# Performance work log

Measured on AMD Instinct MI355X. Metric: run time of the kernel, lower is better.

Reference implementation:

```python
import jax, jax.numpy as jnp
import numpy as np

TOP_K = 2
EPS = 1e-6

def setup_inputs() -> dict:
    key = jax.random.key(0)
    ks = jax.random.split(key, 4)
    B, L, D, E, ED = 2, 2048, 2048, 8, 2048
    scale_gu = (6.0 / D) ** 0.5   # kaiming_uniform-ish bound
    scale_dn = (6.0 / ED) ** 0.5
    return {
        "x": jax.random.normal(ks[0], (B, L, D), jnp.float32),
        "router_scale": jnp.ones((D,), jnp.float32),
        "gate_w": jax.random.normal(ks[1], (D, E), jnp.float32) * (D ** -0.5),
        "gate_up": jax.random.uniform(ks[2], (E, D, 2 * ED), jnp.float32, -scale_gu, scale_gu),
        "down": jax.random.uniform(ks[3], (E, ED, D), jnp.float32, -scale_dn, scale_dn),
        "per_expert_scale": jnp.ones((E,), jnp.float32),
    }

def reference(x, router_scale, gate_w, gate_up, down, per_expert_scale):
    B, L, D = x.shape
    E = gate_up.shape[0]
    # --- Router: RMSNorm (no scale) * D^-0.5 * router_scale -> linear -> softmax -> topk -> renorm
    h = x * jax.lax.rsqrt(jnp.mean(x * x, axis=-1, keepdims=True) + EPS)
    h = h * (D ** -0.5) * router_scale
    logits = (h @ gate_w).astype(jnp.float32)            # [B,L,E]
    probs = jax.nn.softmax(logits, axis=-1)
    w, idx = jax.lax.top_k(probs, TOP_K)                 # [B,L,K]
    w = w / jnp.clip(jnp.sum(w, axis=-1, keepdims=True), 1e-12)
    w = w.astype(x.dtype)
    # --- Experts: dense compute over all experts, weighted combine by routing
    N = B * L
    xf = x.reshape(N, D)
    idxf = idx.reshape(N, TOP_K)
    wf = w.reshape(N, TOP_K)
    # combine[n,e] = sum_k wf[n,k] * (idxf[n,k]==e); top_k indices are distinct per token
    combine = jnp.zeros((N, E), x.dtype).at[jnp.arange(N)[:, None], idxf].add(wf)
    hh = jnp.einsum('nd,edf->nef', xf, gate_up)          # [N,E,2*ED]
    gate, up = jnp.split(hh, 2, axis=-1)
    act = jax.nn.gelu(gate, approximate=False) * up      # [N,E,ED]
    y = jnp.einsum('nef,efd->ned', act, down)            # [N,E,D]
    out = jnp.einsum('ne,ned->nd', combine * per_expert_scale, y)
    return out.reshape(B, L, D)
```

## Files before the change

### kernel.cpp

```cpp
#include <hip/hip_runtime.h>
#include <hip/hip_bf16.h>
#include <math.h>

#define NTOK 4096
#define DM   2048
#define NE   8
#define BK   64

using f32x4  = float __attribute__((ext_vector_type(4)));
using bf16x8 = __bf16 __attribute__((ext_vector_type(8)));
using u32x4  = unsigned int __attribute__((ext_vector_type(4)));

__device__ __forceinline__ unsigned short bf16bits(float f){
  unsigned u = __builtin_bit_cast(unsigned, f);
  return (unsigned short)((u + 0x7fffu + ((u >> 16) & 1u)) >> 16);
}

__device__ __forceinline__ void load_lds16(const void* g, void* l){
  __builtin_amdgcn_global_load_lds(
      (const __attribute__((address_space(1))) unsigned int*)g,
      (__attribute__((address_space(3))) unsigned int*)l, 16, 0, 0);
}

__global__ __launch_bounds__(256) void router_kernel(
    const float* __restrict__ x, const float* __restrict__ rs,
    const float* __restrict__ gw, const float* __restrict__ pes,
    unsigned short* __restrict__ xbf, int* __restrict__ cnt,
    int* __restrict__ toklist, float* __restrict__ slotw)
{
  const int wv = threadIdx.x >> 6, l = threadIdx.x & 63;
  const int n = blockIdx.x * 4 + wv;
  const float* xr = x + (size_t)n * DM;
  unsigned short* xb = xbf + (size_t)n * DM;
  float ssq = 0.f;
  float lg[8] = {0,0,0,0,0,0,0,0};
  #pragma unroll
  for (int q = 0; q < 8; ++q){
    int c4 = l + 64 * q;
    float4 v = ((const float4*)xr)[c4];
    float4 r = ((const float4*)rs)[c4];
    ssq += v.x*v.x + v.y*v.y + v.z*v.z + v.w*v.w;
    ushort4 o; o.x = bf16bits(v.x); o.y = bf16bits(v.y); o.z = bf16bits(v.z); o.w = bf16bits(v.w);
    ((ushort4*)xb)[c4] = o;
    float xs0 = v.x*r.x, xs1 = v.y*r.y, xs2 = v.z*r.z, xs3 = v.w*r.w;
    const float4* gp = (const float4*)(gw + (size_t)c4 * 32);
    float4 ga, gb;
    ga = gp[0]; gb = gp[1];
    lg[0]+=xs0*ga.x; lg[1]+=xs0*ga.y; lg[2]+=xs0*ga.z; lg[3]+=xs0*ga.w;
    lg[4]+=xs0*gb.x; lg[5]+=xs0*gb.y; lg[6]+=xs0*gb.z; lg[7]+=xs0*gb.w;
    ga = gp[2]; gb = gp[3];
    lg[0]+=xs1*ga.x; lg[1]+=xs1*ga.y; lg[2]+=xs1*ga.z; lg[3]+=xs1*ga.w;
    lg[4]+=xs1*gb.x; lg[5]+=xs1*gb.y; lg[6]+=xs1*gb.z; lg[7]+=xs1*gb.w;
    ga = gp[4]; gb = gp[5];
    lg[0]+=xs2*ga.x; lg[1]+=xs2*ga.y; lg[2]+=xs2*ga.z; lg[3]+=xs2*ga.w;
    lg[4]+=xs2*gb.x; lg[5]+=xs2*gb.y; lg[6]+=xs2*gb.z; lg[7]+=xs2*gb.w;
    ga = gp[6]; gb = gp[7];
    lg[0]+=xs3*ga.x; lg[1]+=xs3*ga.y; lg[2]+=xs3*ga.z; lg[3]+=xs3*ga.w;
    lg[4]+=xs3*gb.x; lg[5]+=xs3*gb.y; lg[6]+=xs3*gb.z; lg[7]+=xs3*gb.w;
  }
  #pragma unroll
  for (int off = 32; off; off >>= 1){
    ssq += __shfl_xor(ssq, off, 64);
    #pragma unroll
    for (int e2 = 0; e2 < 8; ++e2) lg[e2] += __shfl_xor(lg[e2], off, 64);
  }
  if (l == 0){
    float c = rsqrtf(ssq * (1.0f/DM) + 1e-6f) * 0.022097086912079608f;
    float mx = -1e30f;
    #pragma unroll
    for (int e2 = 0; e2 < 8; ++e2){ lg[e2] *= c; mx = fmaxf(mx, lg[e2]); }
    float l0 = lg[0]; int i0 = 0;
    #pragma unroll
    for (int e2 = 1; e2 < 8; ++e2) if (lg[e2] > l0){ l0 = lg[e2]; i0 = e2; }
    int i1 = (i0 == 0) ? 1 : 0; float l1 = (i0 == 0) ? lg[1] : lg[0];
    #pragma unroll
    for (int e2 = 0; e2 < 8; ++e2){ if (e2 != i0 && lg[e2] > l1){ l1 = lg[e2]; i1 = e2; } }
    float p0 = expf(l0 - mx), p1 = expf(l1 - mx);
    float sw = fmaxf(p0 + p1, 1e-12f);
    float w0 = p0 / sw, w1 = p1 / sw;
    int s0 = atomicAdd(&cnt[i0], 1);
    toklist[i0 * NTOK + s0] = n;
    slotw[i0 * NTOK + s0] = w0 * pes[i0];
    int s1 = atomicAdd(&cnt[i1], 1);
    toklist[i1 * NTOK + s1] = n;
    slotw[i1 * NTOK + s1] = w1 * pes[i1];
  }
}

__global__ void scan_kernel(const int* __restrict__ cnt, int* __restrict__ basep){
  if (threadIdx.x == 0){
    int a = 0;
    for (int e = 0; e < NE; ++e){ basep[e] = a; a += cnt[e]; }
  }
}

__global__ __launch_bounds__(256) void conv_transpose_kernel(
    const float* __restrict__ W, unsigned short* __restrict__ Wt, int ncols)
{
  const int z = blockIdx.z;
  const float* src = W + (size_t)z * 2048 * ncols;
  unsigned short* dst = Wt + (size_t)z * ncols * 2048;
  const int n0 = blockIdx.x * 64, k0 = blockIdx.y * 64;
  __shared__ __align__(16) unsigned short t[64][72];
  const int tid = threadIdx.x;
  const int kl = tid >> 4;
  const int nl = (tid & 15) * 4;
  #pragma unroll
  for (int q = 0; q < 4; ++q){
    int k = kl + q * 16;
    float4 v = *(const float4*)(src + (size_t)(k0 + k) * ncols + n0 + nl);
    t[nl+0][k] = bf16bits(v.x);
    t[nl+1][k] = bf16bits(v.y);
    t[nl+2][k] = bf16bits(v.z);
    t[nl+3][k] = bf16bits(v.w);
  }
  __syncthreads();
  const int nr = tid >> 3;
  const int k8 = (tid & 7) * 8;
  #pragma unroll
  for (int q = 0; q < 2; ++q){
    int n = nr + q * 32;
    u32x4 v = *(const u32x4*)&t[n][k8];
    *(u32x4*)(dst + (size_t)(n0 + n) * 2048 + k0 + k8) = v;
  }
}

template<int MODE>
__global__ __launch_bounds__(256, 4) void moe_gemm(
    const unsigned short* __restrict__ Abuf,
    const unsigned short* __restrict__ Wt,
    unsigned short* __restrict__ act,
    float* __restrict__ out,
    const int* __restrict__ cnt,
    const int* __restrict__ basep,
    const int* __restrict__ toklist,
    const float* __restrict__ slotw,
    int e0)
{
  int e, fbi, m0;
  if (gridDim.z == NE){
    int flat = blockIdx.x + gridDim.x * (blockIdx.y + 32 * blockIdx.z);
    e = e0 + (flat & 7);
    int Mreal = (cnt[e] + 127) >> 7;
    int j = flat >> 3;
    if (j >= Mreal * (int)gridDim.x) return;
    m0 = (j % Mreal) * 128;
    fbi = j / Mreal;
  } else {
    e = e0 + blockIdx.z;
    m0 = blockIdx.y * 128;
    fbi = blockIdx.x;
  }
  const int z = e - e0;
  const int ce = cnt[e];
  if (m0 >= ce) return;
  const int tid = threadIdx.x;
  const int l = tid & 63;
  const int wv = tid >> 6;
  const int wr = wv >> 1, wc = wv & 1;
  const int baseE = basep[e];
  const size_t ncols = (MODE == 0) ? 4096 : 2048;
  const unsigned short* Wz = Wt + (size_t)z * ncols * 2048;

  __shared__ __align__(16) unsigned short As[128 * BK];
  __shared__ __align__(16) unsigned short Bs[128 * BK];
  __shared__ unsigned char diagpad[MODE ? 544 : 16];
  if (basep[0] == -1) *(volatile unsigned char*)&diagpad[tid & 15] = 1;

  const unsigned short* asrc[4];
  const unsigned short* bsrc[4];
  #pragma unroll
  for (int q = 0; q < 4; ++q){
    int row = q * 32 + (tid >> 3);
    int g = (tid & 7) ^ (row & 7);
    long rs;
    if (MODE == 0) rs = toklist[e * NTOK + min(m0 + row, ce - 1)];
    else           rs = baseE + min(m0 + row, ce - 1);
    asrc[q] = Abuf + (size_t)rs * 2048 + g * 8;
    int wcol;
    if (MODE == 0) wcol = (row < 64) ? (fbi * 64 + row) : (2048 + fbi * 64 + row - 64);
    else           wcol = fbi * 128 + row;
    bsrc[q] = Wz + (size_t)wcol * 2048 + g * 8;
  }

  f32x4 acc[4][4];
  #pragma unroll
  for (int i = 0; i < 4; ++i)
    #pragma unroll
    for (int j2 = 0; j2 < 4; ++j2)
      acc[i][j2] = (f32x4){0.f, 0.f, 0.f, 0.f};

  const int aoff0 = (wr * 64 + (l & 15)) * BK;
  int boffs[4];
  if (MODE == 0){
    boffs[0] = (wc * 32 + (l & 15)) * BK;
    boffs[1] = (wc * 32 + 16 + (l & 15)) * BK;
    boffs[2] = (64 + wc * 32 + (l & 15)) * BK;
    boffs[3] = (64 + wc * 32 + 16 + (l & 15)) * BK;
  } else {
    #pragma unroll
    for (int ni = 0; ni < 4; ++ni) boffs[ni] = (wc * 64 + ni * 16 + (l & 15)) * BK;
  }
  const int lsw = l & 7;
  const int lq = l >> 4;

  #pragma unroll 1
  for (int k0 = 0; k0 < 2048; k0 += BK){
    if (k0) __syncthreads();
    #pragma unroll
    for (int q = 0; q < 4; ++q)
      load_lds16(asrc[q] + k0, &As[q * 2048 + wv * 512]);
    #pragma unroll
    for (int q = 0; q < 4; ++q)
      load_lds16(bsrc[q] + k0, &Bs[q * 2048 + wv * 512]);
    __syncthreads();
    #pragma unroll
    for (int kk = 0; kk < 2; ++kk){
      const int gsw = ((kk * 4 + lq) ^ lsw) * 8;
      bf16x8 af[4];
      #pragma unroll
      for (int mi = 0; mi < 4; ++mi)
        af[mi] = *(const bf16x8*)&As[aoff0 + mi * 16 * BK + gsw];
      #pragma unroll
      for (int ni = 0; ni < 4; ++ni){
        bf16x8 bfr = *(const bf16x8*)&Bs[boffs[ni] + gsw];
        #pragma unroll
        for (int mi = 0; mi < 4; ++mi)
          acc[mi][ni] = __builtin_amdgcn_mfma_f32_16x16x32_bf16(
              af[mi], bfr, acc[mi][ni], 0, 0, 0);
      }
    }
  }

  const int lq4 = (l >> 4) * 4;
  if (MODE == 0){
    #pragma unroll
    for (int mi = 0; mi < 4; ++mi)
      #pragma unroll
      for (int j2 = 0; j2 < 4; ++j2){
        int s = m0 + wr * 64 + mi * 16 + lq4 + j2;
        if (s < ce){
          size_t rowb = (size_t)(baseE + s) * 2048;
          #pragma unroll
          for (int p = 0; p < 2; ++p){
            float g = acc[mi][p][j2];
            float u = acc[mi][p + 2][j2];
            float a = 0.5f * g * (1.0f + erff(g * 0.70710678118654752f)) * u;
            act[rowb + fbi * 64 + wc * 32 + p * 16 + (l & 15)] = bf16bits(a);
          }
        }
      }
  } else {
    #pragma unroll
    for (int mi = 0; mi < 4; ++mi)
      #pragma unroll
      for (int j2 = 0; j2 < 4; ++j2){
        int s = m0 + wr * 64 + mi * 16 + lq4 + j2;
        if (s < ce){
          int tokn = toklist[e * NTOK + s];
          float wgt = slotw[e * NTOK + s];
          float* orow = out + (size_t)tokn * 2048 + fbi * 128 + wc * 64 + (l & 15);
          #pragma unroll
          for (int ni = 0; ni < 4; ++ni)
            atomicAdd(&orow[ni * 16], wgt * acc[mi][ni][j2]);
        }
      }
  }
}

extern "C" void kernel_launch(void* const* d_in, const int* in_sizes, int n_in,
                              void* d_out, int out_size, void* d_ws, size_t ws_size,
                              hipStream_t stream)
{
  const float* x   = (const float*)d_in[0];
  const float* rs  = (const float*)d_in[1];
  const float* gw  = (const float*)d_in[2];
  const float* w1  = (const float*)d_in[3];
  const float* w2  = (const float*)d_in[4];
  const float* pes = (const float*)d_in[5];
  float* out = (float*)d_out;

  char* ws = (char*)d_ws;
  int*   cnt      = (int*)ws;
  int*   basep    = (int*)(ws + 64);
  int*   toklist  = (int*)(ws + 256);
  float* slotw    = (float*)(ws + 256 + (size_t)NE * NTOK * 4);
  unsigned short* xbf  = (unsigned short*)(ws + 256 + 2 * (size_t)NE * NTOK * 4);
  unsigned short* act  = xbf + (size_t)NTOK * DM;
  unsigned short* wtb  = act + (size_t)2 * NTOK * DM;

  const size_t fixed = (size_t)((char*)wtb - ws);
  const size_t per_e = (size_t)4096 * 2048 * 2;

  hipMemsetAsync(out, 0, (size_t)out_size * sizeof(float), stream);
  hipMemsetAsync(cnt, 0, 64, stream);
  router_kernel<<<NTOK / 4, 256, 0, stream>>>(x, rs, gw, pes, xbf, cnt, toklist, slotw);
  scan_kernel<<<1, 64, 0, stream>>>(cnt, basep);

  if (ws_size >= fixed + (size_t)NE * per_e){
    conv_transpose_kernel<<<dim3(64, 32, NE), 256, 0, stream>>>(w1, wtb, 4096);
    moe_gemm<0><<<dim3(32, 32, NE), 256, 0, stream>>>(
        xbf, wtb, act, out, cnt, basep, toklist, slotw, 0);
    conv_transpose_kernel<<<dim3(32, 32, NE), 256, 0, stream>>>(w2, wtb, 2048);
    moe_gemm<1><<<dim3(16, 32, NE), 256, 0, stream>>>(
        act, wtb, act, out, cnt, basep, toklist, slotw, 0);
  } else {
    int EG = (int)((ws_size > fixed) ? ((ws_size - fixed) / per_e) : 0);
    if (EG < 1) EG = 1;
    if (EG > NE) EG = NE;
    for (int g = 0; g < NE; g += EG){
      int gg = min(EG, NE - g);
      conv_transpose_kernel<<<dim3(64, 32, gg), 256, 0, stream>>>(
          w1 + (size_t)g * 2048 * 4096, wtb, 4096);
      moe_gemm<0><<<dim3(32, 32, gg), 256, 0, stream>>>(
          xbf, wtb, act, out, cnt, basep, toklist, slotw, g);
    }
    for (int g = 0; g < NE; g += EG){
      int gg = min(EG, NE - g);
      conv_transpose_kernel<<<dim3(32, 32, gg), 256, 0, stream>>>(
          w2 + (size_t)g * 2048 * 2048, wtb, 2048);
      moe_gemm<1><<<dim3(16, 32, gg), 256, 0, stream>>>(
          act, wtb, act, out, cnt, basep, toklist, slotw, g);
    }
  }
}
```

Before: 522.2 us.

## Split-K down GEMM into bf16 buffers and combine per token without atomics

The down-projection GEMM now splits K in two, doubling grid blocks, and writes bf16 partial expert outputs to a workspace buffer instead of atomically adding into the output. A new combine kernel gathers each token's two expert rows and both K halves, applies the routing weights and writes the output directly, so the output memset is no longer needed on the main path. The flattened expert-interleaved block scheduling is also removed. In exchange this adds extra global traffic for the intermediate buffer and another launch, and rounding partials to bf16 before summing loses precision.

New measurement: 485.3 us. 1.08x faster.

```diff
diff --git a/kernel.cpp b/kernel.cpp
--- a/kernel.cpp
+++ b/kernel.cpp
@@ -16,6 +16,9 @@
   return (unsigned short)((u + 0x7fffu + ((u >> 16) & 1u)) >> 16);
 }
 
+__device__ __forceinline__ float bflo(unsigned u){ return __builtin_bit_cast(float, u << 16); }
+__device__ __forceinline__ float bfhi(unsigned u){ return __builtin_bit_cast(float, u & 0xffff0000u); }
+
 __device__ __forceinline__ void load_lds16(const void* g, void* l){
   __builtin_amdgcn_global_load_lds(
       (const __attribute__((address_space(1))) unsigned int*)g,
@@ -26,7 +29,8 @@
     const float* __restrict__ x, const float* __restrict__ rs,
     const float* __restrict__ gw, const float* __restrict__ pes,
     unsigned short* __restrict__ xbf, int* __restrict__ cnt,
-    int* __restrict__ toklist, float* __restrict__ slotw)
+    int* __restrict__ toklist, float* __restrict__ slotw,
+    int* __restrict__ tok2slot)
 {
   const int wv = threadIdx.x >> 6, l = threadIdx.x & 63;
   const int n = blockIdx.x * 4 + wv;
@@ -81,9 +85,11 @@
     int s0 = atomicAdd(&cnt[i0], 1);
     toklist[i0 * NTOK + s0] = n;
     slotw[i0 * NTOK + s0] = w0 * pes[i0];
+    tok2slot[2 * n] = (i0 << 16) | s0;
     int s1 = atomicAdd(&cnt[i1], 1);
     toklist[i1 * NTOK + s1] = n;
     slotw[i1 * NTOK + s1] = w1 * pes[i1];
+    tok2slot[2 * n + 1] = (i1 << 16) | s1;
   }
 }
 
@@ -131,29 +137,20 @@
     const unsigned short* __restrict__ Wt,
     unsigned short* __restrict__ act,
     float* __restrict__ out,
+    unsigned short* __restrict__ ybuf,
     const int* __restrict__ cnt,
     const int* __restrict__ basep,
     const int* __restrict__ toklist,
     const float* __restrict__ slotw,
     int e0)
 {
-  int e, fbi, m0;
-  if (gridDim.z == NE){
-    int flat = blockIdx.x + gridDim.x * (blockIdx.y + 32 * blockIdx.z);
-    e = e0 + (flat & 7);
-    int Mreal = (cnt[e] + 127) >> 7;
-    int j = flat >> 3;
-    if (j >= Mreal * (int)gridDim.x) return;
-    m0 = (j % Mreal) * 128;
-    fbi = j / Mreal;
-  } else {
-    e = e0 + blockIdx.z;
-    m0 = blockIdx.y * 128;
-    fbi = blockIdx.x;
-  }
-  const int z = e - e0;
+  const int z = blockIdx.z, e = e0 + z;
   const int ce = cnt[e];
+  int my = blockIdx.y, ks = 0;
+  if (MODE == 1){ ks = my & 1; my >>= 1; }
+  const int m0 = my * 128;
   if (m0 >= ce) return;
+  const int fbi = blockIdx.x;
   const int tid = threadIdx.x;
   const int l = tid & 63;
   const int wv = tid >> 6;
@@ -164,7 +161,7 @@
 
   __shared__ __align__(16) unsigned short As[128 * BK];
   __shared__ __align__(16) unsigned short Bs[128 * BK];
-  __shared__ unsigned char diagpad[MODE ? 544 : 16];
+  __shared__ unsigned char diagpad[MODE == 0 ? 16 : (MODE == 1 ? 544 : 1056)];
   if (basep[0] == -1) *(volatile unsigned char*)&diagpad[tid & 15] = 1;
 
   const unsigned short* asrc[4];
@@ -204,9 +201,12 @@
   const int lsw = l & 7;
   const int lq = l >> 4;
 
+  const int kbeg = (MODE == 1) ? ks * 1024 : 0;
+  const int kend = (MODE == 1) ? kbeg + 1024 : 2048;
+
   #pragma unroll 1
-  for (int k0 = 0; k0 < 2048; k0 += BK){
-    if (k0) __syncthreads();
+  for (int k0 = kbeg; k0 < kend; k0 += BK){
+    if (k0 != kbeg) __syncthreads();
     #pragma unroll
     for (int q = 0; q < 4; ++q)
       load_lds16(asrc[q] + k0, &As[q * 2048 + wv * 512]);
@@ -250,6 +250,20 @@
           }
         }
       }
+  } else if (MODE == 1){
+    unsigned short* yb = ybuf + (size_t)ks * (2 * NTOK) * 2048;
+    #pragma unroll
+    for (int mi = 0; mi < 4; ++mi)
+      #pragma unroll
+      for (int j2 = 0; j2 < 4; ++j2){
+        int s = m0 + wr * 64 + mi * 16 + lq4 + j2;
+        if (s < ce){
+          unsigned short* yr = yb + (size_t)(baseE + s) * 2048 + fbi * 128 + wc * 64 + (l & 15);
+          #pragma unroll
+          for (int ni = 0; ni < 4; ++ni)
+            yr[ni * 16] = bf16bits(acc[mi][ni][j2]);
+        }
+      }
   } else {
     #pragma unroll
     for (int mi = 0; mi < 4; ++mi)
@@ -268,6 +282,41 @@
   }
 }
 
+__global__ __launch_bounds__(256) void combine_kernel(
+    const unsigned short* __restrict__ ybuf, const int* __restrict__ tok2slot,
+    const float* __restrict__ slotw, const int* __restrict__ basep,
+    float* __restrict__ out)
+{
+  const int n = blockIdx.x * 4 + (threadIdx.x >> 6);
+  const int l = threadIdx.x & 63;
+  const size_t KS = (size_t)(2 * NTOK) * 2048;
+  int p0 = tok2slot[2 * n], p1 = tok2slot[2 * n + 1];
+  int e0 = p0 >> 16, s0 = p0 & 0xffff;
+  int e1 = p1 >> 16, s1 = p1 & 0xffff;
+  float w0 = slotw[e0 * NTOK + s0], w1 = slotw[e1 * NTOK + s1];
+  const unsigned short* ya = ybuf + (size_t)(basep[e0] + s0) * 2048;
+  const unsigned short* yb = ybuf + (size_t)(basep[e1] + s1) * 2048;
+  float* o = out + (size_t)n * 2048;
+  #pragma unroll
+  for (int q = 0; q < 4; ++q){
+    int c8 = (l + 64 * q) * 8;
+    u32x4 a0 = *(const u32x4*)(ya + c8);
+    u32x4 a1 = *(const u32x4*)(ya + KS + c8);
+    u32x4 b0 = *(const u32x4*)(yb + c8);
+    u32x4 b1 = *(const u32x4*)(yb + KS + c8);
+    float rr[8];
+    #pragma unroll
+    for (int i = 0; i < 4; ++i){
+      rr[2*i]   = w0 * (bflo(a0[i]) + bflo(a1[i])) + w1 * (bflo(b0[i]) + bflo(b1[i]));
+      rr[2*i+1] = w0 * (bfhi(a0[i]) + bfhi(a1[i])) + w1 * (bfhi(b0[i]) + bfhi(b1[i]));
+    }
+    float4 v0 = {rr[0], rr[1], rr[2], rr[3]};
+    float4 v1 = {rr[4], rr[5], rr[6], rr[7]};
+    *(float4*)(o + c8) = v0;
+    *(float4*)(o + c8 + 4) = v1;
+  }
+}
+
 extern "C" void kernel_launch(void* const* d_in, const int* in_sizes, int n_in,
                               void* d_out, int out_size, void* d_ws, size_t ws_size,
                               hipStream_t stream)
@@ -285,26 +334,29 @@
   int*   basep    = (int*)(ws + 64);
   int*   toklist  = (int*)(ws + 256);
   float* slotw    = (float*)(ws + 256 + (size_t)NE * NTOK * 4);
-  unsigned short* xbf  = (unsigned short*)(ws + 256 + 2 * (size_t)NE * NTOK * 4);
+  int*   tok2slot = (int*)(ws + 256 + 2 * (size_t)NE * NTOK * 4);
+  unsigned short* xbf  = (unsigned short*)(ws + 256 + 2 * (size_t)NE * NTOK * 4 + (size_t)NTOK * 8);
   unsigned short* act  = xbf + (size_t)NTOK * DM;
   unsigned short* wtb  = act + (size_t)2 * NTOK * DM;
+  unsigned short* ybuf = wtb + (size_t)NE * 2048 * 2048;
 
   const size_t fixed = (size_t)((char*)wtb - ws);
   const size_t per_e = (size_t)4096 * 2048 * 2;
 
-  hipMemsetAsync(out, 0, (size_t)out_size * sizeof(float), stream);
   hipMemsetAsync(cnt, 0, 64, stream);
-  router_kernel<<<NTOK / 4, 256, 0, stream>>>(x, rs, gw, pes, xbf, cnt, toklist, slotw);
+  router_kernel<<<NTOK / 4, 256, 0, stream>>>(x, rs, gw, pes, xbf, cnt, toklist, slotw, tok2slot);
   scan_kernel<<<1, 64, 0, stream>>>(cnt, basep);
 
   if (ws_size >= fixed + (size_t)NE * per_e){
     conv_transpose_kernel<<<dim3(64, 32, NE), 256, 0, stream>>>(w1, wtb, 4096);
     moe_gemm<0><<<dim3(32, 32, NE), 256, 0, stream>>>(
-        xbf, wtb, act, out, cnt, basep, toklist, slotw, 0);
+        xbf, wtb, act, out, ybuf, cnt, basep, toklist, slotw, 0);
     conv_transpose_kernel<<<dim3(32, 32, NE), 256, 0, stream>>>(w2, wtb, 2048);
-    moe_gemm<1><<<dim3(16, 32, NE), 256, 0, stream>>>(
-        act, wtb, act, out, cnt, basep, toklist, slotw, 0);
+    moe_gemm<1><<<dim3(16, 64, NE), 256, 0, stream>>>(
+        act, wtb, act, out, ybuf, cnt, basep, toklist, slotw, 0);
+    combine_kernel<<<NTOK / 4, 256, 0, stream>>>(ybuf, tok2slot, slotw, basep, out);
   } else {
+    hipMemsetAsync(out, 0, (size_t)out_size * sizeof(float), stream);
     int EG = (int)((ws_size > fixed) ? ((ws_size - fixed) / per_e) : 0);
     if (EG < 1) EG = 1;
     if (EG > NE) EG = NE;
@@ -313,14 +365,14 @@
       conv_transpose_kernel<<<dim3(64, 32, gg), 256, 0, stream>>>(
           w1 + (size_t)g * 2048 * 4096, wtb, 4096);
       moe_gemm<0><<<dim3(32, 32, gg), 256, 0, stream>>>(
-          xbf, wtb, act, out, cnt, basep, toklist, slotw, g);
+          xbf, wtb, act, out, ybuf, cnt, basep, toklist, slotw, g);
     }
     for (int g = 0; g < NE; g += EG){
       int gg = min(EG, NE - g);
       conv_transpose_kernel<<<dim3(32, 32, gg), 256, 0, stream>>>(
           w2 + (size_t)g * 2048 * 2048, wtb, 2048);
-      moe_gemm<1><<<dim3(16, 32, gg), 256, 0, stream>>>(
-          act, wtb, act, out, cnt, basep, toklist, slotw, g);
+      moe_gemm<2><<<dim3(16, 32, gg), 256, 0, stream>>>(
+          act, wtb, act, out, ybuf, cnt, basep, toklist, slotw, g);
     }
   }
 }
```
